# Kernel tuning notes

Hardware: AMD Instinct MI355X
Metric: run time of the kernel (lower is better)

The kernel has to match this reference:

```python
import jax, jax.numpy as jnp
import numpy as np

B, T = 64, 4096
K = 67            # 25 body + 21 + 21 hand keypoints
D = 256           # first_layer_size
C = 7             # num_classes
THR = 0.1         # confidence_threshold
EPS = 1e-5        # BatchNorm eps


def setup_inputs() -> dict:
    key = jax.random.key(0)
    ks = jax.random.split(key, 8)
    body = jax.random.normal(ks[0], (B, T, 75), dtype=jnp.float32)
    hand_right = jax.random.normal(ks[1], (B, T, 63), dtype=jnp.float32)
    hand_left = jax.random.normal(ks[2], (B, T, 63), dtype=jnp.float32)
    length = jax.random.randint(ks[3], (B,), 1, T + 1, dtype=jnp.int64)
    W1 = jax.random.normal(ks[4], (2 * K, D), dtype=jnp.float32) * 0.05
    b1 = jnp.zeros((D,), dtype=jnp.float32)
    gamma = jnp.ones((D,), dtype=jnp.float32)
    beta = jnp.zeros((D,), dtype=jnp.float32)
    Wc = jax.random.normal(ks[5], (D, C), dtype=jnp.float32) * 0.05
    bc = jnp.zeros((C,), dtype=jnp.float32)
    return {"body": body, "hand_right": hand_right, "hand_left": hand_left,
            "length": length, "W1": W1, "b1": b1, "gamma": gamma,
            "beta": beta, "Wc": Wc, "bc": bc}


def reference(body, hand_right, hand_left, length, W1, b1, gamma, beta, Wc, bc):
    # concat keypoint streams -> [B, T, 3K] -> [B, T, K, 3]
    feats = jnp.concatenate([body, hand_right, hand_left], axis=2)
    feats = feats.reshape(feats.shape[0], feats.shape[1], -1, 3)
    x, y, conf = feats[..., 0], feats[..., 1], feats[..., 2]
    conf = (conf > THR).astype(feats.dtype)
    # gate coords by confidence, flatten to [B, T, 2K]
    pos = jnp.stack([x * conf, y * conf], axis=3)
    pos = pos.reshape(pos.shape[0], pos.shape[1], -1)
    # static MLP: Linear + ReLU -> [B, T, D]
    sf = jax.nn.relu(jnp.einsum("btf,fd->btd", pos, W1) + b1)
    # masked max pool over valid timesteps (vectorized segment-max)
    mask = jnp.arange(sf.shape[1])[None, :] < length[:, None]      # [B, T]
    pooled = jnp.max(jnp.where(mask[:, :, None], sf, -jnp.inf), axis=1)  # [B, D]
    # BatchNorm1d (training mode: batch statistics)
    mean = pooled.mean(axis=0)
    var = pooled.var(axis=0)
    bn = (pooled - mean) / jnp.sqrt(var + EPS) * gamma + beta
    # classifier
    return bn @ Wc + bc
```

## Files before the change

### kernel.cpp

```cpp
#include <hip/hip_runtime.h>
#include <hip/hip_bf16.h>

#define B_   64
#define T_   4096
#define F_   134
#define FP_  160
#define D_   256
#define C_   7
#define THR_ 0.1f
#define EPS_ 1e-5f
#define NQ_  16

typedef __bf16 bf16x8 __attribute__((ext_vector_type(8)));
typedef float  f32x4  __attribute__((ext_vector_type(4)));

typedef __attribute__((address_space(1))) const unsigned int guint;
typedef __attribute__((address_space(3))) unsigned int luint;

#define FBAR() asm volatile("s_waitcnt vmcnt(0) lgkmcnt(0)\n\ts_barrier" ::: "memory")
#define LBAR() asm volatile("s_waitcnt lgkmcnt(0)\n\ts_barrier" ::: "memory")


__global__ void convert_w1(const float* __restrict__ W1, __bf16* __restrict__ W1bf) {
    __shared__ float tile[32][33];
    const int d0 = blockIdx.x * 32, f0 = blockIdx.y * 32;
    const int tx = threadIdx.x & 31, ty = threadIdx.x >> 5;
#pragma unroll
    for (int r = 0; r < 32; r += 8) {
        int f = f0 + ty + r;
        tile[ty + r][tx] = (f < F_) ? W1[f * D_ + d0 + tx] : 0.f;
    }
    __syncthreads();
#pragma unroll
    for (int r = 0; r < 32; r += 8) {
        int d = d0 + ty + r;
        W1bf[d * FP_ + f0 + tx] = (__bf16)tile[tx][ty + r];
    }
}

__global__ __launch_bounds__(256, 2)
void fused_mlp_pool(const float* __restrict__ body,
                    const float* __restrict__ hr,
                    const float* __restrict__ hl,
                    const int*   __restrict__ length,
                    const float* __restrict__ b1,
                    const __bf16* __restrict__ W1bf,
                    float* __restrict__ pooled)
{
    const int p = blockIdx.x;
    const int q = p >> 6;
    const int r = p & 63;

    const int tid  = threadIdx.x;
    const int wave = tid >> 6;
    const int lane = tid & 63;
    const int quad = lane >> 4;
    const int l16  = lane & 15;
    const int dbase = wave * 64;

    const int L1 = length[1];
    unsigned int mask = 0;
    unsigned long long len01 = 0, len23 = 0;
#pragma unroll
    for (int i = 0; i < 8; i++) {
        int bi = (r + i) & 63;
        int li = (L1 == 0) ? length[2 * bi] : length[bi];
        int ji = q + 16 * i;
        if (ji * 32 < li) mask |= (1u << i);
        if (i < 4) len01 |= (unsigned long long)(unsigned)li << (16 * i);
        else       len23 |= (unsigned long long)(unsigned)li << (16 * (i - 4));
    }
    const int m = __popc(mask);
    if (m == 0) return;

    __shared__ __align__(16) float  raw[2][6432];
    __shared__ __align__(16) __bf16 As2[2][5120];

    const long rowstride = (long)T_;

    auto stage = [&](int c, int bufi) {
        const int  bb = (r + c) & 63;
        const long t0 = (long)(q + 16 * c) * 32;
        const float* bodyt = body + (bb * rowstride + t0) * 75;
        const float* hrt   = hr   + (bb * rowstride + t0) * 63;
        const float* hlt   = hl   + (bb * rowstride + t0) * 63;
        char* rw = (char*)raw[bufi];
        for (int i = wave; i < 10; i += 4) {
            int off = i * 256 + lane * 4;
            if (off < 2400)
                __builtin_amdgcn_global_load_lds((guint*)(bodyt + off),
                                                 (luint*)(rw + off * 4), 16, 0, 0);
        }
        for (int i = wave; i < 8; i += 4) {
            int off = i * 256 + lane * 4;
            if (off < 2016) {
                __builtin_amdgcn_global_load_lds((guint*)(hrt + off),
                                                 (luint*)(rw + 9600 + off * 4), 16, 0, 0);
                __builtin_amdgcn_global_load_lds((guint*)(hlt + off),
                                                 (luint*)(rw + 17664 + off * 4), 16, 0, 0);
            }
        }
    };

    auto nth = [&](int n) -> int {
        unsigned int t = mask;
        for (int k = 0; k < n; k++) t &= t - 1;
        return __ffs(t) - 1;
    };

    int cs  = nth(0);
    int cs1 = (m > 1) ? nth(1) : -1;
    stage(cs, 0);
    if (m > 1) stage(cs1, 1);

    bf16x8 bfrag[4][5];
    float  b1v[4];
#pragma unroll
    for (int n = 0; n < 4; n++) {
        int d = dbase + n * 16 + l16;
        const __bf16* wp = W1bf + d * FP_ + quad * 8;
#pragma unroll
        for (int kt = 0; kt < 5; kt++)
            bfrag[n][kt] = *(const bf16x8*)(wp + kt * 32);
        b1v[n] = b1[d];
    }

    int roffv[8], wv[8];
    {
        const int t  = ((tid >> 5) & 3) * 8 + ((tid >> 2) & 7);
        const int kb = ((tid >> 7) & 1) * 4 + (tid & 3);
#pragma unroll
        for (int it = 0; it < 8; it++) {
            int k = it * 8 + kb;
            roffv[it] = (k < 25) ? t * 75 + 3 * k
                       : (k < 46) ? 2400 + t * 63 + 3 * (k - 25)
                                  : 4416 + t * 63 + 3 * (k - 46);
            wv[it] = ((t >> 4) * 5 + (k >> 4)) * 256
                   + (((k >> 2) & 3) * 16 + (t & 15)) * 4 + (k & 3);
        }
    }
    int roff_c = 0, w_c = 0;
    if (tid < 96) {
        int t = tid & 31, k = 64 + (tid >> 5);
        roff_c = 4416 + t * 63 + 3 * (k - 46);
        w_c = ((t >> 4) * 5 + (k >> 4)) * 256
            + (((k >> 2) & 3) * 16 + (t & 15)) * 4 + (k & 3);
    }

    for (int i = tid; i < 832; i += 256) {
        int bufi = (i >= 416);
        int ii = i - bufi * 416;
        int t = ii & 31, kp = 67 + (ii >> 5);
        int w = ((t >> 4) * 5 + (kp >> 4)) * 256
              + (((kp >> 2) & 3) * 16 + (t & 15)) * 4 + (kp & 3);
        ((unsigned int*)As2[bufi])[w] = 0u;
    }

    auto repack = [&](int bufi) {
        const float* rw = raw[bufi];
        __bf16* A = As2[bufi];
#pragma unroll
        for (int it = 0; it < 8; it++) {
            float x = rw[roffv[it]], y = rw[roffv[it] + 1], cf = rw[roffv[it] + 2];
            bool g = cf > THR_;
            unsigned short ux = __builtin_bit_cast(unsigned short, (__bf16)(g ? x : 0.f));
            unsigned short uy = __builtin_bit_cast(unsigned short, (__bf16)(g ? y : 0.f));
            ((unsigned int*)A)[wv[it]] = (unsigned int)ux | ((unsigned int)uy << 16);
        }
        if (tid < 96) {
            float x = rw[roff_c], y = rw[roff_c + 1], cf = rw[roff_c + 2];
            bool g = cf > THR_;
            unsigned short ux = __builtin_bit_cast(unsigned short, (__bf16)(g ? x : 0.f));
            unsigned short uy = __builtin_bit_cast(unsigned short, (__bf16)(g ? y : 0.f));
            ((unsigned int*)A)[w_c] = (unsigned int)ux | ((unsigned int)uy << 16);
        }
    };

    FBAR();
    repack(0);
    LBAR();

    for (int s = 0; s < m; s++) {
        const int  bufc = s & 1;
        const bool hn   = (s + 1 < m);
        const bool hn2  = (s + 2 < m);
        int cs2 = -1;
        if (hn2) {
            cs2 = cs1 + 1 + (__ffs(mask >> (cs1 + 1)) - 1);
            stage(cs2, bufc);
        }

        if (hn) repack(bufc ^ 1);

        __builtin_amdgcn_s_setprio(1);
        f32x4 acc[2][4];
#pragma unroll
        for (int mm = 0; mm < 2; mm++)
#pragma unroll
            for (int n = 0; n < 4; n++)
                acc[mm][n] = (f32x4){0.f, 0.f, 0.f, 0.f};
#pragma unroll
        for (int kt = 0; kt < 5; kt++) {
#pragma unroll
            for (int mm = 0; mm < 2; mm++) {
                bf16x8 a = *(const bf16x8*)(As2[bufc] + (mm * 5 + kt) * 512 + lane * 8);
#pragma unroll
                for (int n = 0; n < 4; n++)
                    acc[mm][n] = __builtin_amdgcn_mfma_f32_16x16x32_bf16(a, bfrag[n][kt], acc[mm][n], 0, 0, 0);
            }
        }
        __builtin_amdgcn_s_setprio(0);

        const int bb   = (r + cs) & 63;
        const int lenb = (int)((cs < 4 ? (len01 >> (cs * 16))
                                       : (len23 >> ((cs - 4) * 16))) & 0xFFFFull);
        const int tt0  = (q + 16 * cs) * 32;
        float rmax[4] = {0.f, 0.f, 0.f, 0.f};
#pragma unroll
        for (int mm = 0; mm < 2; mm++) {
            int trow0 = tt0 + mm * 16 + quad * 4;
#pragma unroll
            for (int rr = 0; rr < 4; rr++) {
                bool valid = (trow0 + rr) < lenb;
#pragma unroll
                for (int n = 0; n < 4; n++) {
                    float v = acc[mm][n][rr] + b1v[n];
                    v = (v > 0.f) ? v : 0.f;
                    rmax[n] = (valid && v > rmax[n]) ? v : rmax[n];
                }
            }
        }
#pragma unroll
        for (int n = 0; n < 4; n++) {
            rmax[n] = fmaxf(rmax[n], __shfl_xor(rmax[n], 16, 64));
            rmax[n] = fmaxf(rmax[n], __shfl_xor(rmax[n], 32, 64));
        }
        float rsel = (quad == 0) ? rmax[0] : (quad == 1) ? rmax[1]
                   : (quad == 2) ? rmax[2] : rmax[3];

        if (hn) FBAR();

        atomicMax((unsigned int*)(pooled + bb * D_ + tid),
                  __float_as_uint(rsel));

        cs = cs1; cs1 = cs2;
    }
}

__global__ void bn_classifier(const float* __restrict__ pooled,
                              const float* __restrict__ gamma,
                              const float* __restrict__ beta,
                              const float* __restrict__ Wc,
                              const float* __restrict__ bc,
                              float* __restrict__ out)
{
    __shared__ float scale_s[D_], shift_s[D_];
    const int tid = threadIdx.x;
    float s = 0.f, ss = 0.f;
#pragma unroll 8
    for (int b = 0; b < B_; b++) {
        float v = pooled[b * D_ + tid];
        s += v; ss += v * v;
    }
    float mean = s * (1.f / B_);
    float var  = ss * (1.f / B_) - mean * mean;
    var = fmaxf(var, 0.f);
    float sc = gamma[tid] * rsqrtf(var + EPS_);
    scale_s[tid] = sc;
    shift_s[tid] = beta[tid] - mean * sc;

    const int wv = tid >> 6, ln = tid & 63;
    float wcr[4][C_];
#pragma unroll
    for (int j = 0; j < 4; j++)
#pragma unroll
        for (int c = 0; c < C_; c++)
            wcr[j][c] = Wc[(ln * 4 + j) * C_ + c];
    __syncthreads();

    for (int b = wv * 16; b < wv * 16 + 16; b++) {
        float4 v = *(const float4*)(pooled + b * D_ + ln * 4);
        float q[4];
        q[0] = v.x * scale_s[ln * 4 + 0] + shift_s[ln * 4 + 0];
        q[1] = v.y * scale_s[ln * 4 + 1] + shift_s[ln * 4 + 1];
        q[2] = v.z * scale_s[ln * 4 + 2] + shift_s[ln * 4 + 2];
        q[3] = v.w * scale_s[ln * 4 + 3] + shift_s[ln * 4 + 3];
        float p[C_];
#pragma unroll
        for (int c = 0; c < C_; c++) p[c] = 0.f;
#pragma unroll
        for (int j = 0; j < 4; j++)
#pragma unroll
            for (int c = 0; c < C_; c++)
                p[c] += q[j] * wcr[j][c];
#pragma unroll
        for (int c = 0; c < C_; c++) {
#pragma unroll
            for (int off = 1; off < 64; off <<= 1)
                p[c] += __shfl_xor(p[c], off, 64);
        }
        if (ln == 0) {
#pragma unroll
            for (int c = 0; c < C_; c++)
                out[b * C_ + c] = p[c] + bc[c];
        }
    }
}

extern "C" void kernel_launch(void* const* d_in, const int* in_sizes, int n_in,
                              void* d_out, int out_size, void* d_ws, size_t ws_size,
                              hipStream_t stream) {
    const float* body   = (const float*)d_in[0];
    const float* hr     = (const float*)d_in[1];
    const float* hl     = (const float*)d_in[2];
    const int*   length = (const int*)  d_in[3];
    const float* W1     = (const float*)d_in[4];
    const float* b1     = (const float*)d_in[5];
    const float* gamma  = (const float*)d_in[6];
    const float* beta   = (const float*)d_in[7];
    const float* Wc     = (const float*)d_in[8];
    const float* bc     = (const float*)d_in[9];
    float* out = (float*)d_out;

    float*  pooled = (float*)d_ws;
    __bf16* W1bf   = (__bf16*)((char*)d_ws + 65536);

    hipMemsetAsync(d_ws, 0, 65536, stream);
    convert_w1<<<dim3(8, 5), dim3(256), 0, stream>>>(W1, W1bf);
    fused_mlp_pool<<<dim3(NQ_ * 64), dim3(256), 0, stream>>>(body, hr, hl, length, b1, W1bf, pooled);
    bn_classifier<<<dim3(1), dim3(256), 0, stream>>>(pooled, gamma, beta, Wc, bc, out);
}
```

Before: 233.0 us.

## Restructure chunk pipeline with partial vmcnt waits, fold memset, rewrite classifier

The main kernel now keeps a single bf16 A tile and prefetches only one chunk ahead. Instead of a full memory drain, it waits with partial vmcnt counts so the next chunk's loads overlap repack and MFMA. The separate hipMemsetAsync is removed and pooled is zeroed inside convert_w1, saving a launch. The classifier is rewritten so each thread computes one or two output elements with Wc staged in LDS, replacing the shuffle reductions. Repack now sits on the critical path each iteration, and the hand-tuned vmcnt counts depend on how many loads each wave issues, so a wrong count would read stale data.

```diff
diff --git a/kernel.cpp b/kernel.cpp
--- a/kernel.cpp
+++ b/kernel.cpp
@@ -17,14 +17,17 @@
 typedef __attribute__((address_space(1))) const unsigned int guint;
 typedef __attribute__((address_space(3))) unsigned int luint;
 
-#define FBAR() asm volatile("s_waitcnt vmcnt(0) lgkmcnt(0)\n\ts_barrier" ::: "memory")
-#define LBAR() asm volatile("s_waitcnt lgkmcnt(0)\n\ts_barrier" ::: "memory")
-
-
-__global__ void convert_w1(const float* __restrict__ W1, __bf16* __restrict__ W1bf) {
+#define BARW(N) asm volatile("s_waitcnt vmcnt(" #N ") lgkmcnt(0)\n\ts_barrier" ::: "memory")
+#define LBAR()  asm volatile("s_waitcnt lgkmcnt(0)\n\ts_barrier" ::: "memory")
+
+
+__global__ void convert_w1(const float* __restrict__ W1, __bf16* __restrict__ W1bf,
+                           float* __restrict__ pooled) {
     __shared__ float tile[32][33];
     const int d0 = blockIdx.x * 32, f0 = blockIdx.y * 32;
     const int tx = threadIdx.x & 31, ty = threadIdx.x >> 5;
+    const int gid = (blockIdx.y * 8 + blockIdx.x) * 256 + threadIdx.x;
+    for (int i = gid; i < B_ * D_; i += 40 * 256) pooled[i] = 0.f;
 #pragma unroll
     for (int r = 0; r < 32; r += 8) {
         int f = f0 + ty + r;
@@ -74,16 +77,14 @@
     if (m == 0) return;
 
     __shared__ __align__(16) float  raw[2][6432];
-    __shared__ __align__(16) __bf16 As2[2][5120];
-
-    const long rowstride = (long)T_;
+    __shared__ __align__(16) __bf16 As[10 * 512];
 
     auto stage = [&](int c, int bufi) {
         const int  bb = (r + c) & 63;
         const long t0 = (long)(q + 16 * c) * 32;
-        const float* bodyt = body + (bb * rowstride + t0) * 75;
-        const float* hrt   = hr   + (bb * rowstride + t0) * 63;
-        const float* hlt   = hl   + (bb * rowstride + t0) * 63;
+        const float* bodyt = body + (bb * (long)T_ + t0) * 75;
+        const float* hrt   = hr   + (bb * (long)T_ + t0) * 63;
+        const float* hlt   = hl   + (bb * (long)T_ + t0) * 63;
         char* rw = (char*)raw[bufi];
         for (int i = wave; i < 10; i += 4) {
             int off = i * 256 + lane * 4;
@@ -102,16 +103,9 @@
         }
     };
 
-    auto nth = [&](int n) -> int {
-        unsigned int t = mask;
-        for (int k = 0; k < n; k++) t &= t - 1;
-        return __ffs(t) - 1;
-    };
-
-    int cs  = nth(0);
-    int cs1 = (m > 1) ? nth(1) : -1;
+    int cs  = __ffs(mask) - 1;
+    int cs1 = (m > 1) ? (cs + 1 + (__ffs(mask >> (cs + 1)) - 1)) : -1;
     stage(cs, 0);
-    if (m > 1) stage(cs1, 1);
 
     bf16x8 bfrag[4][5];
     float  b1v[4];
@@ -147,50 +141,47 @@
             + (((k >> 2) & 3) * 16 + (t & 15)) * 4 + (k & 3);
     }
 
-    for (int i = tid; i < 832; i += 256) {
-        int bufi = (i >= 416);
-        int ii = i - bufi * 416;
-        int t = ii & 31, kp = 67 + (ii >> 5);
-        int w = ((t >> 4) * 5 + (kp >> 4)) * 256
-              + (((kp >> 2) & 3) * 16 + (t & 15)) * 4 + (kp & 3);
-        ((unsigned int*)As2[bufi])[w] = 0u;
+    for (int i = tid; i < 416; i += 256) {
+        int tt = i & 31, kp = 67 + (i >> 5);
+        int w = ((tt >> 4) * 5 + (kp >> 4)) * 256
+              + (((kp >> 2) & 3) * 16 + (tt & 15)) * 4 + (kp & 3);
+        ((unsigned int*)As)[w] = 0u;
     }
 
     auto repack = [&](int bufi) {
         const float* rw = raw[bufi];
-        __bf16* A = As2[bufi];
 #pragma unroll
         for (int it = 0; it < 8; it++) {
             float x = rw[roffv[it]], y = rw[roffv[it] + 1], cf = rw[roffv[it] + 2];
             bool g = cf > THR_;
             unsigned short ux = __builtin_bit_cast(unsigned short, (__bf16)(g ? x : 0.f));
             unsigned short uy = __builtin_bit_cast(unsigned short, (__bf16)(g ? y : 0.f));
-            ((unsigned int*)A)[wv[it]] = (unsigned int)ux | ((unsigned int)uy << 16);
+            ((unsigned int*)As)[wv[it]] = (unsigned int)ux | ((unsigned int)uy << 16);
         }
         if (tid < 96) {
             float x = rw[roff_c], y = rw[roff_c + 1], cf = rw[roff_c + 2];
             bool g = cf > THR_;
             unsigned short ux = __builtin_bit_cast(unsigned short, (__bf16)(g ? x : 0.f));
             unsigned short uy = __builtin_bit_cast(unsigned short, (__bf16)(g ? y : 0.f));
-            ((unsigned int*)A)[w_c] = (unsigned int)ux | ((unsigned int)uy << 16);
+            ((unsigned int*)As)[w_c] = (unsigned int)ux | ((unsigned int)uy << 16);
         }
     };
 
-    FBAR();
-    repack(0);
-    LBAR();
-
+    int cur = 0;
     for (int s = 0; s < m; s++) {
-        const int  bufc = s & 1;
-        const bool hn   = (s + 1 < m);
-        const bool hn2  = (s + 2 < m);
-        int cs2 = -1;
-        if (hn2) {
-            cs2 = cs1 + 1 + (__ffs(mask >> (cs1 + 1)) - 1);
-            stage(cs2, bufc);
-        }
-
-        if (hn) repack(bufc ^ 1);
+        const bool hn = (s + 1 < m);
+        if (hn) stage(cs1, cur ^ 1);
+
+        if (s == 0) {
+            if (hn) { if (wave < 2) BARW(7); else BARW(6); }
+            else    BARW(0);
+        } else {
+            if (hn) { if (wave < 2) BARW(8); else BARW(7); }
+            else    BARW(1);
+        }
+
+        repack(cur);
+        LBAR();
 
         __builtin_amdgcn_s_setprio(1);
         f32x4 acc[2][4];
@@ -203,7 +194,7 @@
         for (int kt = 0; kt < 5; kt++) {
 #pragma unroll
             for (int mm = 0; mm < 2; mm++) {
-                bf16x8 a = *(const bf16x8*)(As2[bufc] + (mm * 5 + kt) * 512 + lane * 8);
+                bf16x8 a = *(const bf16x8*)(As + (mm * 5 + kt) * 512 + lane * 8);
 #pragma unroll
                 for (int n = 0; n < 4; n++)
                     acc[mm][n] = __builtin_amdgcn_mfma_f32_16x16x32_bf16(a, bfrag[n][kt], acc[mm][n], 0, 0, 0);
@@ -237,13 +228,12 @@
         }
         float rsel = (quad == 0) ? rmax[0] : (quad == 1) ? rmax[1]
                    : (quad == 2) ? rmax[2] : rmax[3];
-
-        if (hn) FBAR();
-
         atomicMax((unsigned int*)(pooled + bb * D_ + tid),
                   __float_as_uint(rsel));
 
-        cs = cs1; cs1 = cs2;
+        cur ^= 1;
+        cs = cs1;
+        if (s + 2 < m) cs1 = cs + 1 + (__ffs(mask >> (cs + 1)) - 1);
     }
 }
 
@@ -254,7 +244,7 @@
                               const float* __restrict__ bc,
                               float* __restrict__ out)
 {
-    __shared__ float scale_s[D_], shift_s[D_];
+    __shared__ float scale_s[D_], shift_s[D_], Wc_s[D_ * C_];
     const int tid = threadIdx.x;
     float s = 0.f, ss = 0.f;
 #pragma unroll 8
@@ -263,48 +253,34 @@
         s += v; ss += v * v;
     }
     float mean = s * (1.f / B_);
-    float var  = ss * (1.f / B_) - mean * mean;
-    var = fmaxf(var, 0.f);
+    float var  = fmaxf(ss * (1.f / B_) - mean * mean, 0.f);
     float sc = gamma[tid] * rsqrtf(var + EPS_);
     scale_s[tid] = sc;
     shift_s[tid] = beta[tid] - mean * sc;
-
-    const int wv = tid >> 6, ln = tid & 63;
-    float wcr[4][C_];
-#pragma unroll
-    for (int j = 0; j < 4; j++)
-#pragma unroll
-        for (int c = 0; c < C_; c++)
-            wcr[j][c] = Wc[(ln * 4 + j) * C_ + c];
+#pragma unroll
+    for (int i = tid; i < D_ * C_; i += 256) Wc_s[i] = Wc[i];
     __syncthreads();
 
-    for (int b = wv * 16; b < wv * 16 + 16; b++) {
-        float4 v = *(const float4*)(pooled + b * D_ + ln * 4);
-        float q[4];
-        q[0] = v.x * scale_s[ln * 4 + 0] + shift_s[ln * 4 + 0];
-        q[1] = v.y * scale_s[ln * 4 + 1] + shift_s[ln * 4 + 1];
-        q[2] = v.z * scale_s[ln * 4 + 2] + shift_s[ln * 4 + 2];
-        q[3] = v.w * scale_s[ln * 4 + 3] + shift_s[ln * 4 + 3];
-        float p[C_];
-#pragma unroll
-        for (int c = 0; c < C_; c++) p[c] = 0.f;
-#pragma unroll
-        for (int j = 0; j < 4; j++)
-#pragma unroll
-            for (int c = 0; c < C_; c++)
-                p[c] += q[j] * wcr[j][c];
-#pragma unroll
-        for (int c = 0; c < C_; c++) {
-#pragma unroll
-            for (int off = 1; off < 64; off <<= 1)
-                p[c] += __shfl_xor(p[c], off, 64);
-        }
-        if (ln == 0) {
-#pragma unroll
-            for (int c = 0; c < C_; c++)
-                out[b * C_ + c] = p[c] + bc[c];
-        }
-    }
+    const int oi = tid;
+    const int b0 = oi / C_, c0 = oi - b0 * C_;
+    const int oj = tid + 256;
+    const bool has2 = oj < B_ * C_;
+    const int b1i = oj / C_, c1i = oj - b1i * C_;
+    float a0 = bc[c0];
+    float a1 = has2 ? bc[c1i] : 0.f;
+    const float* row0 = pooled + b0 * D_;
+    const float* row1 = pooled + (has2 ? b1i : 0) * D_;
+#pragma unroll 8
+    for (int d = 0; d < D_; d++) {
+        float bn0 = row0[d] * scale_s[d] + shift_s[d];
+        a0 += bn0 * Wc_s[d * C_ + c0];
+        if (has2) {
+            float bn1 = row1[d] * scale_s[d] + shift_s[d];
+            a1 += bn1 * Wc_s[d * C_ + c1i];
+        }
+    }
+    out[oi] = a0;
+    if (has2) out[oj] = a1;
 }
 
 extern "C" void kernel_launch(void* const* d_in, const int* in_sizes, int n_in,
@@ -325,8 +301,7 @@
     float*  pooled = (float*)d_ws;
     __bf16* W1bf   = (__bf16*)((char*)d_ws + 65536);
 
-    hipMemsetAsync(d_ws, 0, 65536, stream);
-    convert_w1<<<dim3(8, 5), dim3(256), 0, stream>>>(W1, W1bf);
+    convert_w1<<<dim3(8, 5), dim3(256), 0, stream>>>(W1, W1bf, pooled);
     fused_mlp_pool<<<dim3(NQ_ * 64), dim3(256), 0, stream>>>(body, hr, hl, length, b1, W1bf, pooled);
     bn_classifier<<<dim3(1), dim3(256), 0, stream>>>(pooled, gamma, beta, Wc, bc, out);
 }
```

After: 255.2 us. +9.5%, slower.
